# Kernel tuning notes

Hardware: AMD Instinct MI355X
Metric: run time of the kernel (lower is better)

## Reference

```python
import jax, jax.numpy as jnp
import numpy as np

ROUTINGS = 4
NUM_CAPSULE = 16
DIM_CAPSULE = 16
EPS = 1e-7  # K.epsilon()
L2_EPS = 1e-12  # tf.nn.l2_normalize epsilon


def squash(x, axis=-1):
    s = jnp.sum(jnp.square(x), axis=axis, keepdims=True) + EPS
    scale = jnp.sqrt(s) / (0.5 + s)
    return scale * x


def l2_normalize(x, axis=-1):
    s = jnp.sum(jnp.square(x), axis=axis, keepdims=True)
    return x * jax.lax.rsqrt(jnp.maximum(s, L2_EPS))


def setup_inputs() -> dict:
    key = jax.random.key(0)
    k1, k2 = jax.random.split(key)
    u_vecs = jax.random.normal(k1, (32, 4096, 128), dtype=jnp.float32)
    # glorot-ish scale for kernel-size-1 conv weight (input_dim=128 -> num_cap*dim_cap=256)
    W = jax.random.normal(k2, (128, 256), dtype=jnp.float32) * 0.05
    return {"u_vecs": u_vecs, "W": W}


def reference(u_vecs, W):
    B, I, _ = u_vecs.shape
    # conv1d with kernel size 1 == pointwise projection
    u_hat = jnp.einsum('bid,dk->bik', u_vecs, W)
    u_hat = u_hat.reshape(B, I, NUM_CAPSULE, DIM_CAPSULE)
    u_hat = jnp.transpose(u_hat, (0, 2, 1, 3))  # [B, N, I, D]

    b = jnp.zeros((B, NUM_CAPSULE, I), dtype=u_hat.dtype)
    o = None
    for i in range(ROUTINGS):
        c = jax.nn.softmax(b, axis=1)  # softmax over output-capsule axis
        o = jnp.einsum('bni,bnid->bnd', c, u_hat)  # [B, N, D]
        if i < ROUTINGS - 1:
            o = l2_normalize(o, axis=-1)
            b = jnp.einsum('bnd,bnid->bni', o, u_hat)  # logits reset each iter
    return squash(o, axis=-1)
```

## Files before the change

### kernel.cpp

```cpp
#include <hip/hip_runtime.h>

#define BATCH 32
#define I_TOT 4096
#define N_CAP 16
#define K_DIM 128

#define CCHUNK 64
#define NCH_CS 64
#define NRCH 32
#define RCHUNK 128

#define WS_CS    0
#define WS_FBWO  262144
#define WS_WOB   327680
#define WS_SP    360448
#define WS_PACKT 2457600
#define WS_TOTAL_F (WS_PACKT + 8388608)

typedef __attribute__((ext_vector_type(8))) short bf16x8;
typedef __attribute__((ext_vector_type(4))) float f32x4;

__device__ inline ushort f2bf(float x) {
    unsigned u = __float_as_uint(x);
    u += 0x7FFFu + ((u >> 16) & 1u);
    return (ushort)(u >> 16);
}

__global__ __launch_bounds__(256) void pack_kernel(const float* __restrict__ u,
                                                   float* __restrict__ ws, int do_pack) {
    const int b = blockIdx.y, chunk = blockIdx.x, t = threadIdx.x;
    const int c0 = chunk * CCHUNK;
    ushort* ut = (ushort*)(ws + WS_PACKT);
    const int k4 = t & 31, rg = t >> 5;

    __shared__ ushort lds_bf[CCHUNK][K_DIM + 8];
    __shared__ __align__(16) float4 red[8][32];

    float4 acc = {0.f, 0.f, 0.f, 0.f};
    #pragma unroll
    for (int m = 0; m < 8; m++) {
        int R = c0 + m * 8 + rg;
        float4 v = *(const float4*)&u[((size_t)b * I_TOT + R) * K_DIM + k4 * 4];
        acc.x += v.x; acc.y += v.y; acc.z += v.z; acc.w += v.w;
        if (do_pack) {
            ushort4 w = { f2bf(v.x), f2bf(v.y), f2bf(v.z), f2bf(v.w) };
            *(ushort4*)&lds_bf[m * 8 + rg][k4 * 4] = w;
        }
    }
    red[rg][k4] = acc;
    __syncthreads();
    if (t < 32) {
        float4 s = red[0][t];
        #pragma unroll
        for (int r = 1; r < 8; r++) {
            float4 v = red[r][t];
            s.x += v.x; s.y += v.y; s.z += v.z; s.w += v.w;
        }
        *(float4*)&ws[WS_CS + ((size_t)(b * NCH_CS + chunk)) * K_DIM + t * 4] = s;
    }

    if (do_pack) {
        __syncthreads();
        #pragma unroll
        for (int q = 0; q < 4; q++) {
            int cc = q * 256 + t;
            int k = cc & 127, io = cc >> 7;
            int ig0 = c0 + io * 8;
            bf16x8 w8;
            #pragma unroll
            for (int j = 0; j < 8; j++) w8[j] = (short)lds_bf[io * 8 + j][k];
            size_t off = ((((size_t)(b * 8 + (k >> 4))) * 128 + (ig0 >> 5)) * 64
                          + (k & 15) + ((io & 3) << 4)) * 8;
            *(bf16x8*)&ut[off] = w8;
        }
    }
}

__global__ __launch_bounds__(128) void update_kernel(const float* __restrict__ W,
                                                     float* __restrict__ ws,
                                                     float* __restrict__ out,
                                                     int mode, int wo_bf16) {
    const int n = blockIdx.x, b = blockIdx.y, t = threadIdx.x;

    __shared__ float s_n[K_DIM];
    __shared__ float o_s[N_CAP + 4];

    if (mode == 0) {
        const float* cs = ws + WS_CS + (size_t)b * NCH_CS * K_DIM;
        float a = 0.f;
        #pragma unroll 16
        for (int c = 0; c < NCH_CS; c++) a += cs[(size_t)c * K_DIM + t];
        s_n[t] = a * (1.f / 16.f);
    } else {
        const float* sp = ws + WS_SP + (size_t)b * NRCH * 2048 + n * K_DIM;
        float a = 0.f;
        #pragma unroll 8
        for (int c = 0; c < NRCH; c++) a += sp[(size_t)c * 2048 + t];
        s_n[t] = a;
    }
    __syncthreads();

    {
        const int d = t >> 3, kseg = t & 7;
        const int col = n * 16 + d;
        float p = 0.f;
        #pragma unroll
        for (int j = 0; j < 16; j++) {
            int k = kseg * 16 + j;
            p += s_n[k] * W[k * 256 + col];
        }
        p += __shfl_xor(p, 1); p += __shfl_xor(p, 2); p += __shfl_xor(p, 4);
        if (kseg == 0) o_s[d] = p;
    }
    __syncthreads();

    float ss = (mode == 2) ? 1e-7f : 0.f;
    #pragma unroll
    for (int d = 0; d < 16; d++) { float v = o_s[d]; ss += v * v; }

    if (mode == 2) {
        if (t < 16) {
            float scale = sqrtf(ss) / (0.5f + ss);
            out[b * 256 + n * 16 + t] = scale * o_s[t];
        }
        return;
    }

    const float inv = rsqrtf(fmaxf(ss, 1e-12f));
    const float4* wrow = (const float4*)(W + t * 256 + n * 16);
    const float4* o4 = (const float4*)o_s;
    float acc = 0.f;
    #pragma unroll
    for (int q = 0; q < 4; q++) {
        float4 w = wrow[q];
        float4 o = o4[q];
        acc += w.x * o.x + w.y * o.y + w.z * o.z + w.w * o.w;
    }
    if (wo_bf16) {
        ((ushort*)(ws + WS_WOB))[(size_t)b * 2048 + n * K_DIM + t] = f2bf(acc * inv);
    } else {
        ws[WS_FBWO + (size_t)b * 2048 + n * K_DIM + t] = acc * inv;
    }
}

__global__ __launch_bounds__(256) void routing_mfma(const float* __restrict__ u,
                                                    float* __restrict__ ws) {
    const int b = blockIdx.y, chunk = blockIdx.x, t = threadIdx.x;
    const int lane = t & 63, wave = t >> 6;
    const short* utp = (const short*)(ws + WS_PACKT);

    __shared__ __align__(16) short wo_bf[N_CAP][144];
    __shared__ __align__(16) ushort c_bf[N_CAP][264];

    {
        const ushort* wob = (const ushort*)(ws + WS_WOB) + (size_t)b * 2048;
        bf16x8 v = *(const bf16x8*)&wob[t * 8];
        *(bf16x8*)&wo_bf[t >> 4][(t & 15) * 8] = v;
    }
    __syncthreads();

    const int cap = lane & 15, hi = lane >> 4;
    bf16x8 bfrag[4];
    #pragma unroll
    for (int kt = 0; kt < 4; kt++)
        bfrag[kt] = *(const bf16x8*)&wo_bf[cap][kt * 32 + hi * 8];

    #pragma unroll
    for (int rr = 0; rr < 2; rr++) {
        const int rt = wave * 2 + rr;
        const int row = chunk * RCHUNK + rt * 16 + cap;
        const float* ubase = u + ((size_t)b * I_TOT + row) * K_DIM + hi * 8;
        f32x4 acc = {0.f, 0.f, 0.f, 0.f};
        #pragma unroll
        for (int kt = 0; kt < 4; kt++) {
            float4 f0 = *(const float4*)(ubase + kt * 32);
            float4 f1 = *(const float4*)(ubase + kt * 32 + 4);
            bf16x8 a;
            a[0] = (short)f2bf(f0.x); a[1] = (short)f2bf(f0.y);
            a[2] = (short)f2bf(f0.z); a[3] = (short)f2bf(f0.w);
            a[4] = (short)f2bf(f1.x); a[5] = (short)f2bf(f1.y);
            a[6] = (short)f2bf(f1.z); a[7] = (short)f2bf(f1.w);
            acc = __builtin_amdgcn_mfma_f32_16x16x32_bf16(a, bfrag[kt], acc, 0, 0, 0);
        }
        #pragma unroll
        for (int r = 0; r < 4; r++) {
            float v = acc[r];
            float mx = v;
            mx = fmaxf(mx, __shfl_xor(mx, 1)); mx = fmaxf(mx, __shfl_xor(mx, 2));
            mx = fmaxf(mx, __shfl_xor(mx, 4)); mx = fmaxf(mx, __shfl_xor(mx, 8));
            float e = __expf(v - mx);
            float sm = e;
            sm += __shfl_xor(sm, 1); sm += __shfl_xor(sm, 2);
            sm += __shfl_xor(sm, 4); sm += __shfl_xor(sm, 8);
            c_bf[cap][rt * 16 + hi * 4 + r] = f2bf(e / sm);
        }
    }
    __syncthreads();

    f32x4 s0 = {0.f, 0.f, 0.f, 0.f}, s1 = {0.f, 0.f, 0.f, 0.f};
    const size_t ut_b = (size_t)b * 8;
    #pragma unroll
    for (int ic = 0; ic < 4; ic++) {
        bf16x8 bfr = *(const bf16x8*)&c_bf[cap][ic * 32 + hi * 8];
        const size_t tile = (size_t)chunk * 4 + ic;
        const short* ab0 = utp + (((ut_b + wave * 2 + 0) * 128 + tile) * 64 + lane) * 8;
        const short* ab1 = utp + (((ut_b + wave * 2 + 1) * 128 + tile) * 64 + lane) * 8;
        bf16x8 a0 = *(const bf16x8*)ab0;
        bf16x8 a1 = *(const bf16x8*)ab1;
        s0 = __builtin_amdgcn_mfma_f32_16x16x32_bf16(a0, bfr, s0, 0, 0, 0);
        s1 = __builtin_amdgcn_mfma_f32_16x16x32_bf16(a1, bfr, s1, 0, 0, 0);
    }
    float* spw = ws + WS_SP + ((size_t)b * NRCH + chunk) * 2048;
    #pragma unroll
    for (int r = 0; r < 4; r++) {
        spw[cap * K_DIM + (wave * 2 + 0) * 16 + hi * 4 + r] = s0[r];
        spw[cap * K_DIM + (wave * 2 + 1) * 16 + hi * 4 + r] = s1[r];
    }
}

__global__ __launch_bounds__(256) void routing_fp32(const float* __restrict__ u,
                                                    float* __restrict__ ws) {
    const int b = blockIdx.y, chunk = blockIdx.x, t = threadIdx.x;
    const int i0 = chunk * RCHUNK;

    __shared__ __align__(16) float wo_s[N_CAP][K_DIM];
    __shared__ __align__(16) float c_s[RCHUNK][N_CAP];

    const float* w_o = ws + WS_FBWO + (size_t)b * 2048;
    #pragma unroll
    for (int j = 0; j < 8; j++) {
        int idx = t + j * 256;
        ((float*)wo_s)[idx] = w_o[idx];
    }
    __syncthreads();

    {
        const int row = t >> 1, h = t & 1;
        const float4* upx = (const float4*)(u + ((size_t)b * I_TOT + i0 + row) * K_DIM + h * 64);
        const float4* wp = (const float4*)&wo_s[0][h * 64];
        float logit[16];
        #pragma unroll
        for (int n = 0; n < 16; n++) logit[n] = 0.f;
        #pragma unroll
        for (int q = 0; q < 16; q++) {
            float4 v = upx[q];
            #pragma unroll
            for (int n = 0; n < 16; n++) {
                float4 w = wp[n * 32 + q];
                logit[n] += v.x * w.x + v.y * w.y + v.z * w.z + v.w * w.w;
            }
        }
        #pragma unroll
        for (int n = 0; n < 16; n++) logit[n] += __shfl_xor(logit[n], 1);
        float m = logit[0];
        #pragma unroll
        for (int n = 1; n < 16; n++) m = fmaxf(m, logit[n]);
        float sum = 0.f;
        #pragma unroll
        for (int n = 0; n < 16; n++) { logit[n] = __expf(logit[n] - m); sum += logit[n]; }
        float inv = 1.f / sum;
        float4* crow = (float4*)&c_s[row][h * 8];
        if (h == 0) {
            crow[0] = make_float4(logit[0]*inv, logit[1]*inv, logit[2]*inv, logit[3]*inv);
            crow[1] = make_float4(logit[4]*inv, logit[5]*inv, logit[6]*inv, logit[7]*inv);
        } else {
            crow[0] = make_float4(logit[8]*inv, logit[9]*inv, logit[10]*inv, logit[11]*inv);
            crow[1] = make_float4(logit[12]*inv, logit[13]*inv, logit[14]*inv, logit[15]*inv);
        }
    }
    __syncthreads();

    const int k4 = t & 31, ng = t >> 5;
    float4 a0 = {0.f,0.f,0.f,0.f}, a1 = {0.f,0.f,0.f,0.f};
    const float4* u2 = (const float4*)(u + ((size_t)b * I_TOT + i0) * K_DIM) + k4;
    #pragma unroll 8
    for (int i = 0; i < RCHUNK; i++) {
        float4 v = u2[(size_t)i * 32];
        float2 c2 = *(const float2*)&c_s[i][ng * 2];
        a0.x += v.x * c2.x; a0.y += v.y * c2.x; a0.z += v.z * c2.x; a0.w += v.w * c2.x;
        a1.x += v.x * c2.y; a1.y += v.y * c2.y; a1.z += v.z * c2.y; a1.w += v.w * c2.y;
    }
    float* sp = ws + WS_SP + ((size_t)b * NRCH + chunk) * 2048;
    *(float4*)&sp[(ng * 2 + 0) * K_DIM + k4 * 4] = a0;
    *(float4*)&sp[(ng * 2 + 1) * K_DIM + k4 * 4] = a1;
}

extern "C" void kernel_launch(void* const* d_in, const int* in_sizes, int n_in,
                              void* d_out, int out_size, void* d_ws, size_t ws_size,
                              hipStream_t stream) {
    const float* u = (const float*)d_in[0];
    const float* W = (const float*)d_in[1];
    float* out = (float*)d_out;
    float* ws = (float*)d_ws;

    const int big = (ws_size >= (size_t)WS_TOTAL_F * 4) ? 1 : 0;

    pack_kernel<<<dim3(NCH_CS, BATCH), 256, 0, stream>>>(u, ws, big);
    update_kernel<<<dim3(N_CAP, BATCH), 128, 0, stream>>>(W, ws, out, 0, big);

    for (int pass = 0; pass < 3; pass++) {
        if (big) routing_mfma<<<dim3(NRCH, BATCH), 256, 0, stream>>>(u, ws);
        else     routing_fp32<<<dim3(NRCH, BATCH), 256, 0, stream>>>(u, ws);
        update_kernel<<<dim3(N_CAP, BATCH), 128, 0, stream>>>(
            W, ws, out, pass == 2 ? 2 : 1, big);
    }
}
```

Baseline: 91.56 us.

## Pre-pack bf16 A-fragments of u once and halve routing chunk size

The pack kernel now also writes u in bf16, laid out row-major in the MFMA A-fragment order. The routing kernel loads these fragments directly instead of re-reading fp32 u and converting it on every one of the three passes, which halves the bytes read for the logit stage. The routing grid doubles to 64 chunks of 64 rows, with one row tile per wave, to raise parallelism and occupancy. The costs are a larger workspace, an extra packed copy written once, and twice as many partial sums for the update kernel to reduce.

```diff
diff --git a/kernel.cpp b/kernel.cpp
--- a/kernel.cpp
+++ b/kernel.cpp
@@ -7,14 +7,17 @@
 
 #define CCHUNK 64
 #define NCH_CS 64
-#define NRCH 32
-#define RCHUNK 128
+#define NRCH 64
+#define RROWS 64
+#define FB_NCHUNK 32
+#define FB_RCHUNK 128
 
 #define WS_CS    0
 #define WS_FBWO  262144
 #define WS_WOB   327680
 #define WS_SP    360448
-#define WS_PACKT 2457600
+#define WS_PACK  4554752
+#define WS_PACKT (WS_PACK + 8388608)
 #define WS_TOTAL_F (WS_PACKT + 8388608)
 
 typedef __attribute__((ext_vector_type(8))) short bf16x8;
@@ -30,6 +33,7 @@
                                                    float* __restrict__ ws, int do_pack) {
     const int b = blockIdx.y, chunk = blockIdx.x, t = threadIdx.x;
     const int c0 = chunk * CCHUNK;
+    ushort* up = (ushort*)(ws + WS_PACK);
     ushort* ut = (ushort*)(ws + WS_PACKT);
     const int k4 = t & 31, rg = t >> 5;
 
@@ -44,7 +48,12 @@
         acc.x += v.x; acc.y += v.y; acc.z += v.z; acc.w += v.w;
         if (do_pack) {
             ushort4 w = { f2bf(v.x), f2bf(v.y), f2bf(v.z), f2bf(v.w) };
-            *(ushort4*)&lds_bf[m * 8 + rg][k4 * 4] = w;
+            int k = k4 * 4;
+            int kt = k >> 5, lane_hi = (k & 31) >> 3, j0 = k & 7;
+            size_t off = (((size_t)(b * 256 + (R >> 4)) * 4 + kt) * 64
+                          + (R & 15) + (lane_hi << 4)) * 8 + j0;
+            *(ushort4*)&up[off] = w;
+            *(ushort4*)&lds_bf[m * 8 + rg][k] = w;
         }
     }
     red[rg][k4] = acc;
@@ -79,7 +88,7 @@
 __global__ __launch_bounds__(128) void update_kernel(const float* __restrict__ W,
                                                      float* __restrict__ ws,
                                                      float* __restrict__ out,
-                                                     int mode, int wo_bf16) {
+                                                     int mode, int wo_bf16, int nch) {
     const int n = blockIdx.x, b = blockIdx.y, t = threadIdx.x;
 
     __shared__ float s_n[K_DIM];
@@ -92,10 +101,10 @@
         for (int c = 0; c < NCH_CS; c++) a += cs[(size_t)c * K_DIM + t];
         s_n[t] = a * (1.f / 16.f);
     } else {
-        const float* sp = ws + WS_SP + (size_t)b * NRCH * 2048 + n * K_DIM;
+        const float* sp = ws + WS_SP + (size_t)b * nch * 2048 + n * K_DIM;
         float a = 0.f;
-        #pragma unroll 8
-        for (int c = 0; c < NRCH; c++) a += sp[(size_t)c * 2048 + t];
+        #pragma unroll 16
+        for (int c = 0; c < nch; c++) a += sp[(size_t)c * 2048 + t];
         s_n[t] = a;
     }
     __syncthreads();
@@ -143,14 +152,14 @@
     }
 }
 
-__global__ __launch_bounds__(256) void routing_mfma(const float* __restrict__ u,
-                                                    float* __restrict__ ws) {
+__global__ __launch_bounds__(256, 8) void routing_mfma(float* __restrict__ ws) {
     const int b = blockIdx.y, chunk = blockIdx.x, t = threadIdx.x;
     const int lane = t & 63, wave = t >> 6;
+    const short* up = (const short*)(ws + WS_PACK);
     const short* utp = (const short*)(ws + WS_PACKT);
 
-    __shared__ __align__(16) short wo_bf[N_CAP][144];
-    __shared__ __align__(16) ushort c_bf[N_CAP][264];
+    __shared__ __align__(16) short wo_bf[N_CAP][136];
+    __shared__ __align__(16) ushort c_bf[N_CAP][72];
 
     {
         const ushort* wob = (const ushort*)(ws + WS_WOB) + (size_t)b * 2048;
@@ -165,21 +174,13 @@
     for (int kt = 0; kt < 4; kt++)
         bfrag[kt] = *(const bf16x8*)&wo_bf[cap][kt * 32 + hi * 8];
 
-    #pragma unroll
-    for (int rr = 0; rr < 2; rr++) {
-        const int rt = wave * 2 + rr;
-        const int row = chunk * RCHUNK + rt * 16 + cap;
-        const float* ubase = u + ((size_t)b * I_TOT + row) * K_DIM + hi * 8;
+    {
+        const int rt_g = chunk * 4 + wave;
         f32x4 acc = {0.f, 0.f, 0.f, 0.f};
+        const short* abase = up + (((size_t)(b * 256 + rt_g)) * 4) * 512 + lane * 8;
         #pragma unroll
         for (int kt = 0; kt < 4; kt++) {
-            float4 f0 = *(const float4*)(ubase + kt * 32);
-            float4 f1 = *(const float4*)(ubase + kt * 32 + 4);
-            bf16x8 a;
-            a[0] = (short)f2bf(f0.x); a[1] = (short)f2bf(f0.y);
-            a[2] = (short)f2bf(f0.z); a[3] = (short)f2bf(f0.w);
-            a[4] = (short)f2bf(f1.x); a[5] = (short)f2bf(f1.y);
-            a[6] = (short)f2bf(f1.z); a[7] = (short)f2bf(f1.w);
+            bf16x8 a = *(const bf16x8*)(abase + kt * 512);
             acc = __builtin_amdgcn_mfma_f32_16x16x32_bf16(a, bfrag[kt], acc, 0, 0, 0);
         }
         #pragma unroll
@@ -192,7 +193,7 @@
             float sm = e;
             sm += __shfl_xor(sm, 1); sm += __shfl_xor(sm, 2);
             sm += __shfl_xor(sm, 4); sm += __shfl_xor(sm, 8);
-            c_bf[cap][rt * 16 + hi * 4 + r] = f2bf(e / sm);
+            c_bf[cap][wave * 16 + hi * 4 + r] = f2bf(e / sm);
         }
     }
     __syncthreads();
@@ -200,9 +201,9 @@
     f32x4 s0 = {0.f, 0.f, 0.f, 0.f}, s1 = {0.f, 0.f, 0.f, 0.f};
     const size_t ut_b = (size_t)b * 8;
     #pragma unroll
-    for (int ic = 0; ic < 4; ic++) {
+    for (int ic = 0; ic < 2; ic++) {
         bf16x8 bfr = *(const bf16x8*)&c_bf[cap][ic * 32 + hi * 8];
-        const size_t tile = (size_t)chunk * 4 + ic;
+        const size_t tile = (size_t)chunk * 2 + ic;
         const short* ab0 = utp + (((ut_b + wave * 2 + 0) * 128 + tile) * 64 + lane) * 8;
         const short* ab1 = utp + (((ut_b + wave * 2 + 1) * 128 + tile) * 64 + lane) * 8;
         bf16x8 a0 = *(const bf16x8*)ab0;
@@ -221,10 +222,10 @@
 __global__ __launch_bounds__(256) void routing_fp32(const float* __restrict__ u,
                                                     float* __restrict__ ws) {
     const int b = blockIdx.y, chunk = blockIdx.x, t = threadIdx.x;
-    const int i0 = chunk * RCHUNK;
+    const int i0 = chunk * FB_RCHUNK;
 
     __shared__ __align__(16) float wo_s[N_CAP][K_DIM];
-    __shared__ __align__(16) float c_s[RCHUNK][N_CAP];
+    __shared__ __align__(16) float c_s[FB_RCHUNK][N_CAP];
 
     const float* w_o = ws + WS_FBWO + (size_t)b * 2048;
     #pragma unroll
@@ -274,13 +275,13 @@
     float4 a0 = {0.f,0.f,0.f,0.f}, a1 = {0.f,0.f,0.f,0.f};
     const float4* u2 = (const float4*)(u + ((size_t)b * I_TOT + i0) * K_DIM) + k4;
     #pragma unroll 8
-    for (int i = 0; i < RCHUNK; i++) {
+    for (int i = 0; i < FB_RCHUNK; i++) {
         float4 v = u2[(size_t)i * 32];
         float2 c2 = *(const float2*)&c_s[i][ng * 2];
         a0.x += v.x * c2.x; a0.y += v.y * c2.x; a0.z += v.z * c2.x; a0.w += v.w * c2.x;
         a1.x += v.x * c2.y; a1.y += v.y * c2.y; a1.z += v.z * c2.y; a1.w += v.w * c2.y;
     }
-    float* sp = ws + WS_SP + ((size_t)b * NRCH + chunk) * 2048;
+    float* sp = ws + WS_SP + ((size_t)b * FB_NCHUNK + chunk) * 2048;
     *(float4*)&sp[(ng * 2 + 0) * K_DIM + k4 * 4] = a0;
     *(float4*)&sp[(ng * 2 + 1) * K_DIM + k4 * 4] = a1;
 }
@@ -294,14 +295,15 @@
     float* ws = (float*)d_ws;
 
     const int big = (ws_size >= (size_t)WS_TOTAL_F * 4) ? 1 : 0;
+    const int nch = big ? NRCH : FB_NCHUNK;
 
     pack_kernel<<<dim3(NCH_CS, BATCH), 256, 0, stream>>>(u, ws, big);
-    update_kernel<<<dim3(N_CAP, BATCH), 128, 0, stream>>>(W, ws, out, 0, big);
+    update_kernel<<<dim3(N_CAP, BATCH), 128, 0, stream>>>(W, ws, out, 0, big, nch);
 
     for (int pass = 0; pass < 3; pass++) {
-        if (big) routing_mfma<<<dim3(NRCH, BATCH), 256, 0, stream>>>(u, ws);
-        else     routing_fp32<<<dim3(NRCH, BATCH), 256, 0, stream>>>(u, ws);
+        if (big) routing_mfma<<<dim3(NRCH, BATCH), 256, 0, stream>>>(ws);
+        else     routing_fp32<<<dim3(FB_NCHUNK, BATCH), 256, 0, stream>>>(u, ws);
         update_kernel<<<dim3(N_CAP, BATCH), 128, 0, stream>>>(
-            W, ws, out, pass == 2 ? 2 : 1, big);
-    }
-}
+            W, ws, out, pass == 2 ? 2 : 1, big, nch);
+    }
+}
```

New measurement: 94.25 us. 2.9% more time.
